# Optimization experiments

Measured on AMD Instinct MI355X. Metric: run time of the kernel, lower is better.

## Reference

```python
import jax, jax.numpy as jnp
import numpy as np

N, D_IN, D_OUT = 100000, 256, 256
R, E, B = 8, 40000, 4
LN_EPS = 1e-5


def setup_inputs() -> dict:
    key = jax.random.key(0)
    ks = jax.random.split(key, 6)
    x = jax.random.normal(ks[0], (N, D_IN), dtype=jnp.float32)
    edge_index = jax.random.randint(ks[1], (R, 2, E), 0, N, dtype=jnp.int64)
    bases = jax.random.normal(ks[2], (B, D_IN, D_OUT), dtype=jnp.float32) * 0.01
    coefficients = jax.random.normal(ks[3], (R, B), dtype=jnp.float32) * 0.01
    bound = 1.0 / np.sqrt(D_IN)
    w_self = jax.random.uniform(ks[4], (D_IN, D_OUT), minval=-bound, maxval=bound, dtype=jnp.float32)
    b_self = jax.random.uniform(ks[5], (D_OUT,), minval=-bound, maxval=bound, dtype=jnp.float32)
    ln_gamma = jnp.ones((D_OUT,), dtype=jnp.float32)
    ln_beta = jnp.zeros((D_OUT,), dtype=jnp.float32)
    return {"x": x, "edge_index": edge_index, "bases": bases,
            "coefficients": coefficients, "w_self": w_self, "b_self": b_self,
            "ln_gamma": ln_gamma, "ln_beta": ln_beta}


def reference(x, edge_index, bases, coefficients, w_self, b_self, ln_gamma, ln_beta):
    n = x.shape[0]
    # self loop
    h = x @ w_self + b_self                                   # (N, D_OUT)
    # basis-composed per-relation weights
    W = jnp.einsum('rb,bio->rio', coefficients, bases)        # (R, D_IN, D_OUT)
    src = edge_index[:, 0]                                    # (R, E)
    dst = edge_index[:, 1]                                    # (R, E)
    msg = jnp.einsum('red,rdo->reo', x[src], W)               # (R, E, D_OUT)
    seg = jax.vmap(lambda d, m: jax.ops.segment_sum(m, d, num_segments=n))(dst, msg)
    deg = jax.vmap(lambda d: jax.ops.segment_sum(jnp.ones(d.shape, x.dtype), d, num_segments=n))(dst)
    deg = jnp.maximum(deg, 1.0)                               # clamp(min=1)
    h = h + (seg / deg[..., None]).sum(axis=0)
    # LayerNorm(SiLU(h)); dropout is identity in eval
    a = jax.nn.silu(h)
    mean = a.mean(axis=-1, keepdims=True)
    var = ((a - mean) ** 2).mean(axis=-1, keepdims=True)
    return (a - mean) * jax.lax.rsqrt(var + LN_EPS) * ln_gamma + ln_beta
```

## Files before the change

### kernel.cpp

```cpp
#include <hip/hip_runtime.h>
#include <hip/hip_bf16.h>

#define N_NODES 100000
#define D 256
#define R_REL 8
#define E_EDGES 40000
#define LN_EPS 1e-5f
#define ETOT (R_REL * E_EDGES)
#define SCAN_CH 1024
#define SCAN_NB ((N_NODES + SCAN_CH - 1) / SCAN_CH)
#define NROWT ((N_NODES + 127) / 128)
#define NWG (NROWT * 10)
#define PREPX_NB (N_NODES * D / 8 / 256)
#define PREPB_NB 80
#define COUNT_NB ((ETOT + 255) / 256)

typedef __attribute__((ext_vector_type(8))) short short8;
typedef __attribute__((ext_vector_type(4))) float f32x4;
typedef __attribute__((ext_vector_type(2))) float f32x2;
typedef unsigned char uchar;

__device__ inline ushort bf16u(float f) {
    __hip_bfloat16 h = __float2bfloat16(f);
    return *reinterpret_cast<ushort*>(&h);
}
__device__ inline float bf2f(ushort u) { return __uint_as_float(((unsigned)u) << 16); }

__global__ __launch_bounds__(256) void k_prep(const float* __restrict__ x,
                                              ushort* __restrict__ xb,
                                              const float* __restrict__ w_self,
                                              const float* __restrict__ bases,
                                              ushort* __restrict__ BT,
                                              const int* __restrict__ ei,
                                              int* __restrict__ cntR) {
    __shared__ float tile[64][65];
    int b = blockIdx.x;
    int t = threadIdx.x;
    if (b < PREPX_NB) {
        size_t idx = (size_t)b * 256 + t;
        const float4* xp = (const float4*)(x + idx * 8);
        float4 f0 = xp[0], f1 = xp[1];
        short8 v;
        v[0] = (short)bf16u(f0.x); v[1] = (short)bf16u(f0.y);
        v[2] = (short)bf16u(f0.z); v[3] = (short)bf16u(f0.w);
        v[4] = (short)bf16u(f1.x); v[5] = (short)bf16u(f1.y);
        v[6] = (short)bf16u(f1.z); v[7] = (short)bf16u(f1.w);
        *(short8*)(xb + idx * 8) = v;
    } else if (b < PREPX_NB + PREPB_NB) {
        int bb = b - PREPX_NB;
        int ot = bb >> 2, dt = bb & 3;
        int o0 = ot * 64, d0 = dt * 64;
        int m = o0 >> 8;
        const float* src = (m == 0) ? w_self : bases + (size_t)(m - 1) * D * D;
        int ol0 = o0 & 255;
        int cl = t & 63, rw = t >> 6;
        for (int i = 0; i < 16; ++i) {
            int dl = i * 4 + rw;
            tile[dl][cl] = src[(size_t)(d0 + dl) * D + ol0 + cl];
        }
        __syncthreads();
        for (int i = 0; i < 16; ++i) {
            int ol = i * 4 + rw;
            BT[(size_t)(o0 + ol) * D + d0 + cl] = bf16u(tile[cl][ol]);
        }
    } else {
        int idx = (b - PREPX_NB - PREPB_NB) * 256 + t;
        if (idx < ETOT) {
            int r = idx / E_EDGES, e = idx % E_EDGES;
            int dst = ei[(r * 2 + 1) * E_EDGES + e];
            atomicAdd(&cntR[(size_t)dst * 8 + r], 1);
        }
    }
}

__global__ __launch_bounds__(256) void k_scanA(const int* __restrict__ cntR,
                                               int* __restrict__ start,
                                               int* __restrict__ sumsA) {
    __shared__ int sc[256];
    int t = threadIdx.x;
    int base = blockIdx.x * SCAN_CH + t * 4;
    int v[4];
#pragma unroll
    for (int i = 0; i < 4; ++i) {
        int node = base + i;
        int s = 0;
        if (node < N_NODES) {
            const int4* c = (const int4*)&cntR[(size_t)node * 8];
            int4 a = c[0], b = c[1];
            s = a.x + a.y + a.z + a.w + b.x + b.y + b.z + b.w;
        }
        v[i] = s;
    }
    int ts = v[0] + v[1] + v[2] + v[3];
    sc[t] = ts;
    __syncthreads();
    for (int off = 1; off < 256; off <<= 1) {
        int val = (t >= off) ? sc[t - off] : 0;
        __syncthreads();
        sc[t] += val;
        __syncthreads();
    }
    int excl = sc[t] - ts;
    if (base + 0 < N_NODES) start[base + 0] = excl;
    if (base + 1 < N_NODES) start[base + 1] = excl + v[0];
    if (base + 2 < N_NODES) start[base + 2] = excl + v[0] + v[1];
    if (base + 3 < N_NODES) start[base + 3] = excl + v[0] + v[1] + v[2];
    if (t == 255) sumsA[blockIdx.x] = sc[255];
}

__global__ __launch_bounds__(256) void k_scanB(const int* __restrict__ sumsA,
                                               int* __restrict__ sumsB) {
    __shared__ int sc[256];
    int t = threadIdx.x;
    int i0 = t * 4;
    int v0 = (i0 + 0 < SCAN_NB) ? sumsA[i0 + 0] : 0;
    int v1 = (i0 + 1 < SCAN_NB) ? sumsA[i0 + 1] : 0;
    int v2 = (i0 + 2 < SCAN_NB) ? sumsA[i0 + 2] : 0;
    int v3 = (i0 + 3 < SCAN_NB) ? sumsA[i0 + 3] : 0;
    int ts = v0 + v1 + v2 + v3;
    sc[t] = ts;
    __syncthreads();
    for (int off = 1; off < 256; off <<= 1) {
        int val = (t >= off) ? sc[t - off] : 0;
        __syncthreads();
        sc[t] += val;
        __syncthreads();
    }
    int excl = sc[t] - ts;
    if (i0 + 0 < SCAN_NB) sumsB[i0 + 0] = excl;
    if (i0 + 1 < SCAN_NB) sumsB[i0 + 1] = excl + v0;
    if (i0 + 2 < SCAN_NB) sumsB[i0 + 2] = excl + v0 + v1;
    if (i0 + 3 < SCAN_NB) sumsB[i0 + 3] = excl + v0 + v1 + v2;
}

__global__ __launch_bounds__(256) void k_scanC(int* __restrict__ start,
                                               const int* __restrict__ sumsB,
                                               int* __restrict__ cursor) {
    int idx = blockIdx.x * blockDim.x + threadIdx.x;
    if (idx < N_NODES) {
        int v = start[idx] + sumsB[idx / SCAN_CH];
        start[idx] = v;
        cursor[idx] = v;
    }
    if (idx == 0) start[N_NODES] = ETOT;
}

__global__ void k_scatter(const int* __restrict__ ei, int* __restrict__ cursor,
                          const int* __restrict__ cntR, int2* __restrict__ pairs) {
    int idx = blockIdx.x * blockDim.x + threadIdx.x;
    if (idx >= ETOT) return;
    int r = idx / E_EDGES, e = idx % E_EDGES;
    int src = ei[r * 2 * E_EDGES + e];
    int dst = ei[(r * 2 + 1) * E_EDGES + e];
    int pos = atomicAdd(&cursor[dst], 1);
    float invd = __builtin_amdgcn_rcpf((float)cntR[(size_t)dst * 8 + r]) * 0.015625f;
    pairs[pos] = make_int2((r << 20) | src, __float_as_int(invd));
}

__global__ __launch_bounds__(256, 2) void k_gemm(const ushort* __restrict__ xb,
                                                 const ushort* __restrict__ BT,
                                                 ushort* __restrict__ hb,
                                                 uchar* __restrict__ U) {
    __shared__ ushort As[2][128 * 64];
    __shared__ ushort Bs[2][128 * 64];
    int t = threadIdx.x;

    const int q = NWG / 8, r8 = NWG % 8;
    int dd = blockIdx.x;
    int xcd = dd & 7, slot = dd >> 3;
    int wgid = (xcd < r8 ? xcd * (q + 1) : r8 * (q + 1) + (xcd - r8) * q) + slot;
    int rowtile = wgid / 10, pass = wgid % 10;
    int row0 = rowtile * 128;

    int l = t & 63, w = t >> 6;
    int wr = w >> 1, wc = w & 1;
    int lr = l & 15, lg = l >> 4;

    auto stageA = [&](int buf, int kt) {
#pragma unroll
        for (int p = 0; p < 4; ++p) {
            int o = p * 4096 + t * 16;
            int rowA = o >> 7;
            int colb = (o & 127) ^ ((rowA & 7) << 4);
            int srcrow = min(row0 + rowA, N_NODES - 1);
            const char* gp = (const char*)xb + ((size_t)srcrow * D + kt * 64) * 2 + colb;
            char* lp = (char*)&As[buf][0] + p * 4096 + (t >> 6) * 1024;
            __builtin_amdgcn_global_load_lds(
                (const __attribute__((address_space(1))) void*)gp,
                (__attribute__((address_space(3))) void*)lp, 16, 0, 0);
        }
    };
    auto stageB = [&](int buf, int kt) {
#pragma unroll
        for (int p = 0; p < 4; ++p) {
            int o = p * 4096 + t * 16;
            int rowB = o >> 7;
            int colb = (o & 127) ^ ((rowB & 7) << 4);
            const char* gp = (const char*)BT +
                ((size_t)(pass * 128 + rowB) * D + kt * 64) * 2 + colb;
            char* lp = (char*)&Bs[buf][0] + p * 4096 + (t >> 6) * 1024;
            __builtin_amdgcn_global_load_lds(
                (const __attribute__((address_space(1))) void*)gp,
                (__attribute__((address_space(3))) void*)lp, 16, 0, 0);
        }
    };

    f32x4 acc[4][4] = {};
    stageA(0, 0); stageB(0, 0);
    stageA(1, 1); stageB(1, 1);
#pragma unroll
    for (int kt = 0; kt < 4; ++kt) {
        int buf = kt & 1;
        if (kt < 3) asm volatile("s_waitcnt vmcnt(8)" ::: "memory");
        else        asm volatile("s_waitcnt vmcnt(0)" ::: "memory");
        __builtin_amdgcn_s_barrier();
        short8 a[2][4], b[2][4];
#pragma unroll
        for (int kk = 0; kk < 2; ++kk) {
            int kb = kk * 64 + lg * 16;
#pragma unroll
            for (int mi = 0; mi < 4; ++mi) {
                int row = wr * 64 + mi * 16 + lr;
                a[kk][mi] = *(const short8*)((const char*)&As[buf][0] +
                             row * 128 + (kb ^ ((row & 7) << 4)));
            }
#pragma unroll
            for (int ni = 0; ni < 4; ++ni) {
                int rb = wc * 64 + ni * 16 + lr;
                b[kk][ni] = *(const short8*)((const char*)&Bs[buf][0] +
                             rb * 128 + (kb ^ ((rb & 7) << 4)));
            }
        }
        asm volatile("s_waitcnt lgkmcnt(0)" ::: "memory");
        __builtin_amdgcn_s_barrier();
        if (kt < 2) { stageA(buf, kt + 2); stageB(buf, kt + 2); }
#pragma unroll
        for (int kk = 0; kk < 2; ++kk)
#pragma unroll
            for (int mi = 0; mi < 4; ++mi)
#pragma unroll
                for (int ni = 0; ni < 4; ++ni)
                    acc[mi][ni] = __builtin_amdgcn_mfma_f32_16x16x32_bf16(
                        a[kk][mi], b[kk][ni], acc[mi][ni], 0, 0, 0);
    }

    if (pass < 2) {
        int qbase = pass * 128 + wc * 64 + lr * 4;
#pragma unroll
        for (int mi = 0; mi < 4; ++mi)
#pragma unroll
            for (int j = 0; j < 4; ++j) {
                int node = row0 + wr * 64 + mi * 16 + lg * 4 + j;
                if (node < N_NODES) {
                    ushort4 v4;
                    v4.x = bf16u(acc[mi][0][j]);
                    v4.y = bf16u(acc[mi][1][j]);
                    v4.z = bf16u(acc[mi][2][j]);
                    v4.w = bf16u(acc[mi][3][j]);
                    *(ushort4*)&hb[(size_t)node * D + qbase] = v4;
                }
            }
    } else {
        int pl = pass - 2;
        int qbase = (pl >> 1) * 256 + (pl & 1) * 128 + wc * 64 + lr * 4;
#pragma unroll
        for (int mi = 0; mi < 4; ++mi)
#pragma unroll
            for (int j = 0; j < 4; ++j) {
                int node = row0 + wr * 64 + mi * 16 + lg * 4 + j;
                if (node < N_NODES) {
                    unsigned d = __builtin_amdgcn_cvt_pk_fp8_f32(
                        acc[mi][0][j] * 64.0f, acc[mi][1][j] * 64.0f, 0, false);
                    d = __builtin_amdgcn_cvt_pk_fp8_f32(
                        acc[mi][2][j] * 64.0f, acc[mi][3][j] * 64.0f, d, true);
                    *(unsigned*)&U[(size_t)node * 1024 + qbase] = d;
                }
            }
    }
}

__global__ __launch_bounds__(256) void k_final(float* __restrict__ out,
                                               const ushort* __restrict__ hb,
                                               const uchar* __restrict__ U,
                                               const int* __restrict__ start,
                                               const int2* __restrict__ pairs,
                                               const float* __restrict__ coeff,
                                               const float* __restrict__ bias,
                                               const float* __restrict__ gamma,
                                               const float* __restrict__ beta) {
    __shared__ float cf[32];
    int t = threadIdx.x;
    if (t < 32) cf[t] = coeff[t];
    __syncthreads();
    int lane = t & 63, w = t >> 6;
    int n = blockIdx.x * 4 + w;
    int s = start[n], e = start[n + 1];

    int c0 = (lane >> 4) * 64 + (lane & 15);
    size_t rowo = (size_t)n * D;
    ushort4 hu = *(const ushort4*)&hb[rowo + lane * 4];
    float bb0 = bias[c0], bb1 = bias[c0 + 16], bb2 = bias[c0 + 32], bb3 = bias[c0 + 48];

    f32x2 a01 = {0.f, 0.f}, a23 = {0.f, 0.f};
    const uchar* Ul = U + lane * 4;
    int p = s;
    for (; p + 1 < e; p += 2) {
        int2 cA = pairs[p], cB = pairs[p + 1];
        const uchar* upA = Ul + ((size_t)(cA.x & 0xFFFFF) << 10);
        const uchar* upB = Ul + ((size_t)(cB.x & 0xFFFFF) << 10);
        unsigned vA0 = *(const unsigned*)(upA);
        unsigned vA1 = *(const unsigned*)(upA + 256);
        unsigned vA2 = *(const unsigned*)(upA + 512);
        unsigned vA3 = *(const unsigned*)(upA + 768);
        unsigned vB0 = *(const unsigned*)(upB);
        unsigned vB1 = *(const unsigned*)(upB + 256);
        unsigned vB2 = *(const unsigned*)(upB + 512);
        unsigned vB3 = *(const unsigned*)(upB + 768);
        float invA = __int_as_float(cA.y);
        float invB = __int_as_float(cB.y);
        const float* wvA = &cf[(cA.x >> 20) * 4];
        const float* wvB = &cf[(cB.x >> 20) * 4];
        f32x2 wp;
        float ww;
        ww = wvA[0] * invA; wp[0] = ww; wp[1] = ww;
        a01 += wp * __builtin_amdgcn_cvt_pk_f32_fp8(vA0, false);
        a23 += wp * __builtin_amdgcn_cvt_pk_f32_fp8(vA0, true);
        ww = wvA[1] * invA; wp[0] = ww; wp[1] = ww;
        a01 += wp * __builtin_amdgcn_cvt_pk_f32_fp8(vA1, false);
        a23 += wp * __builtin_amdgcn_cvt_pk_f32_fp8(vA1, true);
        ww = wvA[2] * invA; wp[0] = ww; wp[1] = ww;
        a01 += wp * __builtin_amdgcn_cvt_pk_f32_fp8(vA2, false);
        a23 += wp * __builtin_amdgcn_cvt_pk_f32_fp8(vA2, true);
        ww = wvA[3] * invA; wp[0] = ww; wp[1] = ww;
        a01 += wp * __builtin_amdgcn_cvt_pk_f32_fp8(vA3, false);
        a23 += wp * __builtin_amdgcn_cvt_pk_f32_fp8(vA3, true);
        ww = wvB[0] * invB; wp[0] = ww; wp[1] = ww;
        a01 += wp * __builtin_amdgcn_cvt_pk_f32_fp8(vB0, false);
        a23 += wp * __builtin_amdgcn_cvt_pk_f32_fp8(vB0, true);
        ww = wvB[1] * invB; wp[0] = ww; wp[1] = ww;
        a01 += wp * __builtin_amdgcn_cvt_pk_f32_fp8(vB1, false);
        a23 += wp * __builtin_amdgcn_cvt_pk_f32_fp8(vB1, true);
        ww = wvB[2] * invB; wp[0] = ww; wp[1] = ww;
        a01 += wp * __builtin_amdgcn_cvt_pk_f32_fp8(vB2, false);
        a23 += wp * __builtin_amdgcn_cvt_pk_f32_fp8(vB2, true);
        ww = wvB[3] * invB; wp[0] = ww; wp[1] = ww;
        a01 += wp * __builtin_amdgcn_cvt_pk_f32_fp8(vB3, false);
        a23 += wp * __builtin_amdgcn_cvt_pk_f32_fp8(vB3, true);
    }
    if (p < e) {
        int2 cA = pairs[p];
        const uchar* upA = Ul + ((size_t)(cA.x & 0xFFFFF) << 10);
        unsigned vA0 = *(const unsigned*)(upA);
        unsigned vA1 = *(const unsigned*)(upA + 256);
        unsigned vA2 = *(const unsigned*)(upA + 512);
        unsigned vA3 = *(const unsigned*)(upA + 768);
        float invA = __int_as_float(cA.y);
        const float* wvA = &cf[(cA.x >> 20) * 4];
        f32x2 wp;
        float ww;
        ww = wvA[0] * invA; wp[0] = ww; wp[1] = ww;
        a01 += wp * __builtin_amdgcn_cvt_pk_f32_fp8(vA0, false);
        a23 += wp * __builtin_amdgcn_cvt_pk_f32_fp8(vA0, true);
        ww = wvA[1] * invA; wp[0] = ww; wp[1] = ww;
        a01 += wp * __builtin_amdgcn_cvt_pk_f32_fp8(vA1, false);
        a23 += wp * __builtin_amdgcn_cvt_pk_f32_fp8(vA1, true);
        ww = wvA[2] * invA; wp[0] = ww; wp[1] = ww;
        a01 += wp * __builtin_amdgcn_cvt_pk_f32_fp8(vA2, false);
        a23 += wp * __builtin_amdgcn_cvt_pk_f32_fp8(vA2, true);
        ww = wvA[3] * invA; wp[0] = ww; wp[1] = ww;
        a01 += wp * __builtin_amdgcn_cvt_pk_f32_fp8(vA3, false);
        a23 += wp * __builtin_amdgcn_cvt_pk_f32_fp8(vA3, true);
    }

    float a[4];
    a[0] = bf2f(hu.x) + bb0 + a01[0];
    a[1] = bf2f(hu.y) + bb1 + a01[1];
    a[2] = bf2f(hu.z) + bb2 + a23[0];
    a[3] = bf2f(hu.w) + bb3 + a23[1];
    float sum = 0.f, sq = 0.f;
#pragma unroll
    for (int j = 0; j < 4; ++j) {
        float ex = __expf(-a[j]);
        a[j] = a[j] * __builtin_amdgcn_rcpf(1.f + ex);
        sum += a[j]; sq += a[j] * a[j];
    }
#pragma unroll
    for (int off = 32; off >= 1; off >>= 1) {
        sum += __shfl_xor(sum, off, 64);
        sq  += __shfl_xor(sq,  off, 64);
    }
    float mean = sum * (1.0f / 256.0f);
    float var = sq * (1.0f / 256.0f) - mean * mean;
    float rs = rsqrtf(var + LN_EPS);
#pragma unroll
    for (int j = 0; j < 4; ++j) {
        int c = c0 + j * 16;
        out[rowo + c] = (a[j] - mean) * rs * gamma[c] + beta[c];
    }
}

extern "C" void kernel_launch(void* const* d_in, const int* in_sizes, int n_in,
                              void* d_out, int out_size, void* d_ws, size_t ws_size,
                              hipStream_t stream) {
    const float* x      = (const float*)d_in[0];
    const int*   ei     = (const int*)d_in[1];
    const float* bases  = (const float*)d_in[2];
    const float* coeff  = (const float*)d_in[3];
    const float* w_self = (const float*)d_in[4];
    const float* b_self = (const float*)d_in[5];
    const float* gamma  = (const float*)d_in[6];
    const float* beta   = (const float*)d_in[7];
    float* out = (float*)d_out;

    ushort* BT  = (ushort*)d_ws;
    ushort* xb  = BT + (size_t)1280 * D;
    ushort* hb  = xb + (size_t)N_NODES * D;
    uchar*  U   = (uchar*)(hb + (size_t)N_NODES * D);
    int* cntR   = (int*)(U + (size_t)N_NODES * 1024);
    int* start  = cntR + (size_t)R_REL * N_NODES;
    int* cursor = start + N_NODES + 1;
    int* sumsA  = cursor + N_NODES;
    int* sumsB  = sumsA + 128;
    int2* pairs = (int2*)(sumsB + 128);

    hipMemsetAsync(cntR, 0, (size_t)R_REL * N_NODES * sizeof(int), stream);

    k_prep<<<PREPX_NB + PREPB_NB + COUNT_NB, 256, 0, stream>>>(x, xb, w_self,
                                                               bases, BT, ei, cntR);
    k_scanA<<<SCAN_NB, 256, 0, stream>>>(cntR, start, sumsA);
    k_scanB<<<1, 256, 0, stream>>>(sumsA, sumsB);
    k_scanC<<<(N_NODES + 255) / 256, 256, 0, stream>>>(start, sumsB, cursor);
    k_scatter<<<(ETOT + 255) / 256, 256, 0, stream>>>(ei, cursor, cntR, pairs);
    k_gemm<<<NWG, 256, 0, stream>>>(xb, BT, hb, U);
    k_final<<<N_NODES / 4, 256, 0, stream>>>(out, hb, U, start, pairs, coeff,
                                             b_self, gamma, beta);
}
```

Baseline: 230.3 us.

## Merge scan kernels, raise MFMA priority, unroll edge gather by four

```diff
diff --git a/kernel.cpp b/kernel.cpp
--- a/kernel.cpp
+++ b/kernel.cpp
@@ -108,37 +108,25 @@
     if (t == 255) sumsA[blockIdx.x] = sc[255];
 }
 
-__global__ __launch_bounds__(256) void k_scanB(const int* __restrict__ sumsA,
-                                               int* __restrict__ sumsB) {
-    __shared__ int sc[256];
+__global__ __launch_bounds__(256) void k_scanC(int* __restrict__ start,
+                                               const int* __restrict__ sumsA,
+                                               int* __restrict__ cursor) {
+    __shared__ int pre[128];
     int t = threadIdx.x;
-    int i0 = t * 4;
-    int v0 = (i0 + 0 < SCAN_NB) ? sumsA[i0 + 0] : 0;
-    int v1 = (i0 + 1 < SCAN_NB) ? sumsA[i0 + 1] : 0;
-    int v2 = (i0 + 2 < SCAN_NB) ? sumsA[i0 + 2] : 0;
-    int v3 = (i0 + 3 < SCAN_NB) ? sumsA[i0 + 3] : 0;
-    int ts = v0 + v1 + v2 + v3;
-    sc[t] = ts;
+    if (t < 128) pre[t] = (t < SCAN_NB) ? sumsA[t] : 0;
     __syncthreads();
-    for (int off = 1; off < 256; off <<= 1) {
-        int val = (t >= off) ? sc[t - off] : 0;
+    for (int off = 1; off < 128; off <<= 1) {
+        int val = 0;
+        if (t < 128 && t >= off) val = pre[t - off];
         __syncthreads();
-        sc[t] += val;
+        if (t < 128) pre[t] += val;
         __syncthreads();
     }
-    int excl = sc[t] - ts;
-    if (i0 + 0 < SCAN_NB) sumsB[i0 + 0] = excl;
-    if (i0 + 1 < SCAN_NB) sumsB[i0 + 1] = excl + v0;
-    if (i0 + 2 < SCAN_NB) sumsB[i0 + 2] = excl + v0 + v1;
-    if (i0 + 3 < SCAN_NB) sumsB[i0 + 3] = excl + v0 + v1 + v2;
-}
-
-__global__ __launch_bounds__(256) void k_scanC(int* __restrict__ start,
-                                               const int* __restrict__ sumsB,
-                                               int* __restrict__ cursor) {
-    int idx = blockIdx.x * blockDim.x + threadIdx.x;
+    int idx = blockIdx.x * blockDim.x + t;
     if (idx < N_NODES) {
-        int v = start[idx] + sumsB[idx / SCAN_CH];
+        int chunk = idx / SCAN_CH;
+        int add = (chunk == 0) ? 0 : pre[chunk - 1];
+        int v = start[idx] + add;
         start[idx] = v;
         cursor[idx] = v;
     }
@@ -234,6 +222,7 @@
         asm volatile("s_waitcnt lgkmcnt(0)" ::: "memory");
         __builtin_amdgcn_s_barrier();
         if (kt < 2) { stageA(buf, kt + 2); stageB(buf, kt + 2); }
+        __builtin_amdgcn_s_setprio(1);
 #pragma unroll
         for (int kk = 0; kk < 2; ++kk)
 #pragma unroll
@@ -242,6 +231,7 @@
                 for (int ni = 0; ni < 4; ++ni)
                     acc[mi][ni] = __builtin_amdgcn_mfma_f32_16x16x32_bf16(
                         a[kk][mi], b[kk][ni], acc[mi][ni], 0, 0, 0);
+        __builtin_amdgcn_s_setprio(0);
     }
 
     if (pass < 2) {
@@ -303,73 +293,77 @@
 
     f32x2 a01 = {0.f, 0.f}, a23 = {0.f, 0.f};
     const uchar* Ul = U + lane * 4;
+
+    auto edgemath = [&](int2 c, unsigned v0, unsigned v1, unsigned v2, unsigned v3) {
+        float inv = __int_as_float(c.y);
+        const float* wv = &cf[(c.x >> 20) * 4];
+        f32x2 wp;
+        float ww;
+        ww = wv[0] * inv; wp[0] = ww; wp[1] = ww;
+        a01 += wp * __builtin_amdgcn_cvt_pk_f32_fp8(v0, false);
+        a23 += wp * __builtin_amdgcn_cvt_pk_f32_fp8(v0, true);
+        ww = wv[1] * inv; wp[0] = ww; wp[1] = ww;
+        a01 += wp * __builtin_amdgcn_cvt_pk_f32_fp8(v1, false);
+        a23 += wp * __builtin_amdgcn_cvt_pk_f32_fp8(v1, true);
+        ww = wv[2] * inv; wp[0] = ww; wp[1] = ww;
+        a01 += wp * __builtin_amdgcn_cvt_pk_f32_fp8(v2, false);
+        a23 += wp * __builtin_amdgcn_cvt_pk_f32_fp8(v2, true);
+        ww = wv[3] * inv; wp[0] = ww; wp[1] = ww;
+        a01 += wp * __builtin_amdgcn_cvt_pk_f32_fp8(v3, false);
+        a23 += wp * __builtin_amdgcn_cvt_pk_f32_fp8(v3, true);
+    };
+
     int p = s;
+    for (; p + 3 < e; p += 4) {
+        int2 cA = pairs[p], cB = pairs[p + 1], cC = pairs[p + 2], cD = pairs[p + 3];
+        const uchar* uA = Ul + ((size_t)(cA.x & 0xFFFFF) << 10);
+        const uchar* uB = Ul + ((size_t)(cB.x & 0xFFFFF) << 10);
+        const uchar* uC = Ul + ((size_t)(cC.x & 0xFFFFF) << 10);
+        const uchar* uD = Ul + ((size_t)(cD.x & 0xFFFFF) << 10);
+        unsigned vA0 = *(const unsigned*)(uA);
+        unsigned vA1 = *(const unsigned*)(uA + 256);
+        unsigned vA2 = *(const unsigned*)(uA + 512);
+        unsigned vA3 = *(const unsigned*)(uA + 768);
+        unsigned vB0 = *(const unsigned*)(uB);
+        unsigned vB1 = *(const unsigned*)(uB + 256);
+        unsigned vB2 = *(const unsigned*)(uB + 512);
+        unsigned vB3 = *(const unsigned*)(uB + 768);
+        unsigned vC0 = *(const unsigned*)(uC);
+        unsigned vC1 = *(const unsigned*)(uC + 256);
+        unsigned vC2 = *(const unsigned*)(uC + 512);
+        unsigned vC3 = *(const unsigned*)(uC + 768);
+        unsigned vD0 = *(const unsigned*)(uD);
+        unsigned vD1 = *(const unsigned*)(uD + 256);
+        unsigned vD2 = *(const unsigned*)(uD + 512);
+        unsigned vD3 = *(const unsigned*)(uD + 768);
+        edgemath(cA, vA0, vA1, vA2, vA3);
+        edgemath(cB, vB0, vB1, vB2, vB3);
+        edgemath(cC, vC0, vC1, vC2, vC3);
+        edgemath(cD, vD0, vD1, vD2, vD3);
+    }
     for (; p + 1 < e; p += 2) {
         int2 cA = pairs[p], cB = pairs[p + 1];
-        const uchar* upA = Ul + ((size_t)(cA.x & 0xFFFFF) << 10);
-        const uchar* upB = Ul + ((size_t)(cB.x & 0xFFFFF) << 10);
-        unsigned vA0 = *(const unsigned*)(upA);
-        unsigned vA1 = *(const unsigned*)(upA + 256);
-        unsigned vA2 = *(const unsigned*)(upA + 512);
-        unsigned vA3 = *(const unsigned*)(upA + 768);
-        unsigned vB0 = *(const unsigned*)(upB);
-        unsigned vB1 = *(const unsigned*)(upB + 256);
-        unsigned vB2 = *(const unsigned*)(upB + 512);
-        unsigned vB3 = *(const unsigned*)(upB + 768);
-        float invA = __int_as_float(cA.y);
-        float invB = __int_as_float(cB.y);
-        const float* wvA = &cf[(cA.x >> 20) * 4];
-        const float* wvB = &cf[(cB.x >> 20) * 4];
-        f32x2 wp;
-        float ww;
-        ww = wvA[0] * invA; wp[0] = ww; wp[1] = ww;
-        a01 += wp * __builtin_amdgcn_cvt_pk_f32_fp8(vA0, false);
-        a23 += wp * __builtin_amdgcn_cvt_pk_f32_fp8(vA0, true);
-        ww = wvA[1] * invA; wp[0] = ww; wp[1] = ww;
-        a01 += wp * __builtin_amdgcn_cvt_pk_f32_fp8(vA1, false);
-        a23 += wp * __builtin_amdgcn_cvt_pk_f32_fp8(vA1, true);
-        ww = wvA[2] * invA; wp[0] = ww; wp[1] = ww;
-        a01 += wp * __builtin_amdgcn_cvt_pk_f32_fp8(vA2, false);
-        a23 += wp * __builtin_amdgcn_cvt_pk_f32_fp8(vA2, true);
-        ww = wvA[3] * invA; wp[0] = ww; wp[1] = ww;
-        a01 += wp * __builtin_amdgcn_cvt_pk_f32_fp8(vA3, false);
-        a23 += wp * __builtin_amdgcn_cvt_pk_f32_fp8(vA3, true);
-        ww = wvB[0] * invB; wp[0] = ww; wp[1] = ww;
-        a01 += wp * __builtin_amdgcn_cvt_pk_f32_fp8(vB0, false);
-        a23 += wp * __builtin_amdgcn_cvt_pk_f32_fp8(vB0, true);
-        ww = wvB[1] * invB; wp[0] = ww; wp[1] = ww;
-        a01 += wp * __builtin_amdgcn_cvt_pk_f32_fp8(vB1, false);
-        a23 += wp * __builtin_amdgcn_cvt_pk_f32_fp8(vB1, true);
-        ww = wvB[2] * invB; wp[0] = ww; wp[1] = ww;
-        a01 += wp * __builtin_amdgcn_cvt_pk_f32_fp8(vB2, false);
-        a23 += wp * __builtin_amdgcn_cvt_pk_f32_fp8(vB2, true);
-        ww = wvB[3] * invB; wp[0] = ww; wp[1] = ww;
-        a01 += wp * __builtin_amdgcn_cvt_pk_f32_fp8(vB3, false);
-        a23 += wp * __builtin_amdgcn_cvt_pk_f32_fp8(vB3, true);
+        const uchar* uA = Ul + ((size_t)(cA.x & 0xFFFFF) << 10);
+        const uchar* uB = Ul + ((size_t)(cB.x & 0xFFFFF) << 10);
+        unsigned vA0 = *(const unsigned*)(uA);
+        unsigned vA1 = *(const unsigned*)(uA + 256);
+        unsigned vA2 = *(const unsigned*)(uA + 512);
+        unsigned vA3 = *(const unsigned*)(uA + 768);
+        unsigned vB0 = *(const unsigned*)(uB);
+        unsigned vB1 = *(const unsigned*)(uB + 256);
+        unsigned vB2 = *(const unsigned*)(uB + 512);
+        unsigned vB3 = *(const unsigned*)(uB + 768);
+        edgemath(cA, vA0, vA1, vA2, vA3);
+        edgemath(cB, vB0, vB1, vB2, vB3);
     }
     if (p < e) {
         int2 cA = pairs[p];
-        const uchar* upA = Ul + ((size_t)(cA.x & 0xFFFFF) << 10);
-        unsigned vA0 = *(const unsigned*)(upA);
-        unsigned vA1 = *(const unsigned*)(upA + 256);
-        unsigned vA2 = *(const unsigned*)(upA + 512);
-        unsigned vA3 = *(const unsigned*)(upA + 768);
-        float invA = __int_as_float(cA.y);
-        const float* wvA = &cf[(cA.x >> 20) * 4];
-        f32x2 wp;
-        float ww;
-        ww = wvA[0] * invA; wp[0] = ww; wp[1] = ww;
-        a01 += wp * __builtin_amdgcn_cvt_pk_f32_fp8(vA0, false);
-        a23 += wp * __builtin_amdgcn_cvt_pk_f32_fp8(vA0, true);
-        ww = wvA[1] * invA; wp[0] = ww; wp[1] = ww;
-        a01 += wp * __builtin_amdgcn_cvt_pk_f32_fp8(vA1, false);
-        a23 += wp * __builtin_amdgcn_cvt_pk_f32_fp8(vA1, true);
-        ww = wvA[2] * invA; wp[0] = ww; wp[1] = ww;
-        a01 += wp * __builtin_amdgcn_cvt_pk_f32_fp8(vA2, false);
-        a23 += wp * __builtin_amdgcn_cvt_pk_f32_fp8(vA2, true);
-        ww = wvA[3] * invA; wp[0] = ww; wp[1] = ww;
-        a01 += wp * __builtin_amdgcn_cvt_pk_f32_fp8(vA3, false);
-        a23 += wp * __builtin_amdgcn_cvt_pk_f32_fp8(vA3, true);
+        const uchar* uA = Ul + ((size_t)(cA.x & 0xFFFFF) << 10);
+        unsigned vA0 = *(const unsigned*)(uA);
+        unsigned vA1 = *(const unsigned*)(uA + 256);
+        unsigned vA2 = *(const unsigned*)(uA + 512);
+        unsigned vA3 = *(const unsigned*)(uA + 768);
+        edgemath(cA, vA0, vA1, vA2, vA3);
     }
 
     float a[4];
@@ -420,16 +414,14 @@
     int* start  = cntR + (size_t)R_REL * N_NODES;
     int* cursor = start + N_NODES + 1;
     int* sumsA  = cursor + N_NODES;
-    int* sumsB  = sumsA + 128;
-    int2* pairs = (int2*)(sumsB + 128);
+    int2* pairs = (int2*)(sumsA + 128);
 
     hipMemsetAsync(cntR, 0, (size_t)R_REL * N_NODES * sizeof(int), stream);
 
     k_prep<<<PREPX_NB + PREPB_NB + COUNT_NB, 256, 0, stream>>>(x, xb, w_self,
                                                                bases, BT, ei, cntR);
     k_scanA<<<SCAN_NB, 256, 0, stream>>>(cntR, start, sumsA);
-    k_scanB<<<1, 256, 0, stream>>>(sumsA, sumsB);
-    k_scanC<<<(N_NODES + 255) / 256, 256, 0, stream>>>(start, sumsB, cursor);
+    k_scanC<<<(N_NODES + 255) / 256, 256, 0, stream>>>(start, sumsA, cursor);
     k_scatter<<<(ETOT + 255) / 256, 256, 0, stream>>>(ei, cursor, cntR, pairs);
     k_gemm<<<NWG, 256, 0, stream>>>(xb, BT, hb, U);
     k_final<<<N_NODES / 4, 256, 0, stream>>>(out, hb, U, start, pairs, coeff,
```

New measurement: 231.2 us (median of 3 runs). No clear change (+0.4%).
